# Kernel tuning notes

Measured on AMD Instinct MI355X. Metric: run time of the kernel, lower is better.

Reference implementation:

```python
import jax, jax.numpy as jnp
import numpy as np
from jax import lax

B, C_IN, H, W = 128, 3, 64, 64
HID = 128          # encoder hidden channels
D = 256            # embedding_dim
K = 1024           # codebook_size
COMMIT = 0.25      # commitment_cost


def conv(x, w, b, stride=2, pad=1):
    # x: NCHW, w: OIHW (torch Conv2d layout)
    y = lax.conv_general_dilated(x, w, (stride, stride), [(pad, pad), (pad, pad)],
                                 dimension_numbers=('NCHW', 'OIHW', 'NCHW'))
    return y + b[None, :, None, None]


def conv_t(x, w, b, stride=2, pad=1):
    # torch ConvTranspose2d: w is (in, out, kh, kw); equivalent to a conv with
    # lhs dilation = stride, flipped kernel, padding k-1-pad.
    k = w.shape[2]
    w_ = jnp.flip(w, (2, 3)).transpose(1, 0, 2, 3)  # -> (out, in, kh, kw)
    p = k - 1 - pad
    y = lax.conv_general_dilated(x, w_, (1, 1), [(p, p), (p, p)],
                                 lhs_dilation=(stride, stride),
                                 dimension_numbers=('NCHW', 'OIHW', 'NCHW'))
    return y + b[None, :, None, None]


def setup_inputs() -> dict:
    key = jax.random.key(0)
    ks = jax.random.split(key, 10)
    s = 0.05
    return {
        'x':        jax.random.normal(ks[0], (B, C_IN, H, W), jnp.float32),
        'enc_w1':   jax.random.normal(ks[1], (HID, C_IN, 4, 4), jnp.float32) * s,
        'enc_b1':   jnp.zeros((HID,), jnp.float32),
        'enc_w2':   jax.random.normal(ks[2], (D, HID, 4, 4), jnp.float32) * s,
        'enc_b2':   jnp.zeros((D,), jnp.float32),
        'dec_w1':   jax.random.normal(ks[3], (D, HID, 4, 4), jnp.float32) * s,   # ConvT: (in,out,kh,kw)
        'dec_b1':   jnp.zeros((HID,), jnp.float32),
        'dec_w2':   jax.random.normal(ks[4], (HID, C_IN, 4, 4), jnp.float32) * s,
        'dec_b2':   jnp.zeros((C_IN,), jnp.float32),
        'codebook': jax.random.normal(ks[5], (K, D), jnp.float32),  # embedding.weight.normal_()
    }


def vqvae_forward(x, enc_w1, enc_b1, enc_w2, enc_b2,
                  dec_w1, dec_b1, dec_w2, dec_b2, codebook):
    # ----- encoder -----
    h = jax.nn.relu(conv(x, enc_w1, enc_b1))          # (B, HID, 32, 32)
    e = conv(h, enc_w2, enc_b2)                        # (B, D, 16, 16)

    # ----- VectorQuantizerEMA.forward (eval mode, no mask) -----
    inputs = e.transpose(0, 2, 3, 1)                   # BCHW -> BHWC
    in_shape = inputs.shape
    flat = inputs.reshape(-1, D)                       # (N, D), N = B*16*16

    # squared L2 distances to every code: (N, K)
    dist = (jnp.sum(flat * flat, axis=1, keepdims=True)
            + jnp.sum(codebook * codebook, axis=1)
            - 2.0 * flat @ codebook.T)

    # max_one_hot(-distances) with straight-through gradients
    logits = -dist
    idx = jnp.argmax(logits, axis=-1)                  # (N,)
    oh = jax.nn.one_hot(idx, K, dtype=logits.dtype)
    flat_oh = oh + logits - lax.stop_gradient(logits)  # values == one-hot

    n_lat = in_shape[1] * in_shape[2]                  # H*W latents
    oh_encodings = flat_oh.reshape(in_shape[0], n_lat, K).transpose(0, 2, 1)  # (B, K, n)

    # quantize under no_grad (torch.no_grad block)
    quantized = lax.stop_gradient(flat_oh @ codebook).reshape(in_shape)

    e_latent_loss = jnp.mean((quantized - inputs) ** 2)
    loss = COMMIT * e_latent_loss

    # straight-through estimator
    quantized = inputs + lax.stop_gradient(quantized - inputs)

    avg_probs = jnp.mean(flat_oh, axis=0)
    perplexity = jnp.exp(-jnp.sum(avg_probs * jnp.log(avg_probs + 1e-10)))

    quantized_nchw = quantized.transpose(0, 3, 1, 2)   # BHWC -> BCHW

    # ----- decoder -----
    d1 = jax.nn.relu(conv_t(quantized_nchw, dec_w1, dec_b1))  # (B, HID, 32, 32)
    x_hat = conv_t(d1, dec_w2, dec_b2)                        # (B, 3, 64, 64)

    return x_hat, loss, perplexity, oh_encodings


def reference(x, enc_w1, enc_b1, enc_w2, enc_b2,
              dec_w1, dec_b1, dec_w2, dec_b2, codebook):
    return vqvae_forward(x, enc_w1, enc_b1, enc_w2, enc_b2,
                         dec_w1, dec_b1, dec_w2, dec_b2, codebook)
```

## Files before the change

### kernel.cpp

```cpp
#include <hip/hip_runtime.h>
#include <stdint.h>

#define NB   128
#define CIN  3
#define HID  128
#define DEM  256
#define KCB  1024
#define NLAT 32768

typedef __bf16 bf16x8 __attribute__((ext_vector_type(8)));
typedef _Float16 f16x8 __attribute__((ext_vector_type(8)));
typedef float  f32x4  __attribute__((ext_vector_type(4)));

__device__ inline unsigned short f2bf(float f) {
    unsigned u = __builtin_bit_cast(unsigned, f);
    u = (u + 0x7fff + ((u >> 16) & 1)) >> 16;
    return (unsigned short)u;
}

__global__ __launch_bounds__(256) void k_zero_oh(float* __restrict__ oh, int n4) {
    int t = blockIdx.x * 256 + threadIdx.x;
    f32x4 z = {0.f, 0.f, 0.f, 0.f};
    for (int i = t; i < n4; i += 256 * 2048)
        __builtin_nontemporal_store(z, (f32x4*)(oh + (size_t)i * 4));
}

__global__ __launch_bounds__(256) void k_conv1(const float* __restrict__ x,
        const float* __restrict__ w, const float* __restrict__ bias,
        unsigned short* __restrict__ hA) {
    __shared__ float sx[3][66][66];
    const int b = blockIdx.y;
    const int ocg = blockIdx.x;
    const int oc0 = ocg * 16;
    const int tid = threadIdx.x;
    for (int i = tid; i < 3 * 66 * 66; i += 256) ((float*)sx)[i] = 0.f;
    __syncthreads();
    const float* xb = x + (size_t)b * (3 * 64 * 64);
    for (int i = tid; i < 3 * 64 * 64; i += 256) {
        int ic = i >> 12; int rem = i & 4095; int y = rem >> 6; int xx = rem & 63;
        sx[ic][y + 1][xx + 1] = xb[i];
    }
    __syncthreads();
    for (int j = 0; j < 4; ++j) {
        int pos = tid + j * 256;
        int oy = pos >> 5, ox = pos & 31;
        float acc[16];
        #pragma unroll
        for (int i = 0; i < 16; ++i) acc[i] = 0.f;
        int iy0 = 2 * oy;
        int ix0 = 2 * ox;
        for (int ic = 0; ic < 3; ++ic) {
            float p[16];
            #pragma unroll
            for (int ky = 0; ky < 4; ++ky)
                #pragma unroll
                for (int kx = 0; kx < 4; ++kx)
                    p[ky * 4 + kx] = sx[ic][iy0 + ky][ix0 + kx];
            #pragma unroll
            for (int oc = 0; oc < 16; ++oc) {
                const float* wp = w + ((oc0 + oc) * 3 + ic) * 16;
                float a = acc[oc];
                #pragma unroll
                for (int t = 0; t < 16; ++t) a = fmaf(p[t], wp[t], a);
                acc[oc] = a;
            }
        }
        unsigned short rec[32];
        #pragma unroll
        for (int oc = 0; oc < 16; ++oc) {
            float v = acc[oc] + bias[oc0 + oc];
            v = v > 0.f ? v : 0.f;
            _Float16 hh = (_Float16)v;
            float hf = (float)hh;
            _Float16 ll = (_Float16)((v - hf) * 2048.0f);
            rec[oc] = __builtin_bit_cast(unsigned short, hh);
            rec[16 + oc] = __builtin_bit_cast(unsigned short, ll);
        }
        uint4* dst = (uint4*)(hA + ((size_t)(b * 8 + ocg) * 1024 + pos) * 32);
        uint4* r4 = (uint4*)rec;
        dst[0] = r4[0]; dst[1] = r4[1]; dst[2] = r4[2]; dst[3] = r4[3];
    }
}

__global__ void k_packwf(const float* __restrict__ w, unsigned short* __restrict__ wpf) {
    int t = blockIdx.x * 256 + threadIdx.x;
    int oc = t >> 7, rest = t & 127;
    int c0 = rest >> 4, ci = rest & 15;
    const float* src = w + ((size_t)(oc * 128 + c0 * 16 + ci)) * 16;
    float tv[16];
    #pragma unroll
    for (int i = 0; i < 16; i += 4) {
        float4 v = *(const float4*)(src + i);
        tv[i] = v.x; tv[i + 1] = v.y; tv[i + 2] = v.z; tv[i + 3] = v.w;
    }
    int g = oc >> 4, lr = oc & 15;
    #pragma unroll
    for (int ks = 0; ks < 8; ++ks) {
        int ky = ks >> 1, kxp = ks & 1;
        #pragma unroll
        for (int kxh = 0; kxh < 2; ++kxh) {
            float v = tv[ky * 4 + 2 * kxp + kxh];
            _Float16 hh = (_Float16)v;
            float hf = (float)hh;
            _Float16 ll = (_Float16)((v - hf) * 2048.0f);
            int d = kxh * 16 + ci;
            int hi = d >> 3, el = d & 7;
            size_t base = ((((size_t)(c0 * 8 + ks) * 16 + g) * 2 + 0) * 4 + hi) * 128 + lr * 8 + el;
            wpf[base]       = __builtin_bit_cast(unsigned short, hh);
            wpf[base + 512] = __builtin_bit_cast(unsigned short, ll);
        }
    }
}

__global__ __launch_bounds__(512) void k_conv2_mfma(const unsigned short* __restrict__ hA,
        const unsigned short* __restrict__ wpf, const float* __restrict__ bias,
        float* __restrict__ e) {
    __shared__ __attribute__((aligned(16))) unsigned short As[577 * 40];
    const int tid = threadIdx.x;
    const int b = blockIdx.y;
    const int ocg = blockIdx.x >> 1, yh = blockIdx.x & 1;
    const int lane = tid & 63, wv = tid >> 6;
    const int wm = wv >> 2, wn = wv & 3;
    const int lr = lane & 15, hi = lane >> 4;

    if (tid < 40) As[576 * 40 + tid] = 0;

    f32x4 acc0[4][2], acc1[4][2];
    #pragma unroll
    for (int i = 0; i < 4; ++i)
        #pragma unroll
        for (int j = 0; j < 2; ++j) {
            acc0[i][j] = (f32x4){0.f, 0.f, 0.f, 0.f};
            acc1[i][j] = (f32x4){0.f, 0.f, 0.f, 0.f};
        }

    for (int c0 = 0; c0 < 8; ++c0) {
        __syncthreads();
        {
            const size_t cbase = (size_t)(b * 8 + c0) * 1024;
            for (int p = tid; p < 2304; p += 512) {
                int l = p >> 7, rem = p & 127;
                int ixs = rem >> 2, q = rem & 3;
                int iy = yh * 16 - 1 + l;
                uint4* dst = (uint4*)(As + (l * 32 + (ixs & 1) * 16 + (ixs >> 1)) * 40 + q * 8);
                if (iy >= 0 && iy < 32)
                    *dst = *(const uint4*)(hA + (cbase + iy * 32 + ixs) * 32 + q * 8);
                else
                    *dst = (uint4){0u, 0u, 0u, 0u};
            }
        }
        __syncthreads();
        #pragma unroll
        for (int ks = 0; ks < 8; ++ks) {
            const int ky = ks >> 1, kxp = ks & 1;
            f16x8 bh[2], bl[2];
            #pragma unroll
            for (int nf = 0; nf < 2; ++nf) {
                const unsigned short* bp = wpf
                    + ((((size_t)(c0 * 8 + ks) * 16 + (ocg * 8 + wn * 2 + nf)) * 2 + 0) * 4 + hi) * 128 + lr * 8;
                bh[nf] = *(const f16x8*)bp;
                bl[nf] = *(const f16x8*)(bp + 512);
            }
            const int o = 2 * kxp - 1 + (hi >> 1);
            const int ix = 2 * lr + o;
            const bool xv = (ix >= 0) && (ix < 32);
            const int sbase = (o & 1) * 16 + (ix >> 1);
            #pragma unroll
            for (int mf = 0; mf < 4; ++mf) {
                int l = 2 * (wm * 4 + mf) + ky;
                int slot = xv ? (l * 32 + sbase) : 576;
                const unsigned short* ap = As + slot * 40 + (hi & 1) * 8;
                f16x8 a0 = *(const f16x8*)ap;
                f16x8 a1 = *(const f16x8*)(ap + 16);
                #pragma unroll
                for (int nf = 0; nf < 2; ++nf) {
                    acc0[mf][nf] = __builtin_amdgcn_mfma_f32_16x16x32_f16(a0, bh[nf], acc0[mf][nf], 0, 0, 0);
                    acc1[mf][nf] = __builtin_amdgcn_mfma_f32_16x16x32_f16(a0, bl[nf], acc1[mf][nf], 0, 0, 0);
                    acc1[mf][nf] = __builtin_amdgcn_mfma_f32_16x16x32_f16(a1, bh[nf], acc1[mf][nf], 0, 0, 0);
                }
            }
        }
    }
    #pragma unroll
    for (int mf = 0; mf < 4; ++mf) {
        int oy = yh * 8 + wm * 4 + mf;
        #pragma unroll
        for (int nf = 0; nf < 2; ++nf) {
            int oc = ocg * 128 + wn * 32 + nf * 16 + lr;
            float bv = bias[oc];
            #pragma unroll
            for (int r = 0; r < 4; ++r) {
                int ox = hi * 4 + r;
                size_t erow = (size_t)b * 256 + (size_t)oy * 16 + ox;
                e[erow * 256 + oc] = acc0[mf][nf][r] + acc1[mf][nf][r] * (1.0f / 2048.0f) + bv;
            }
        }
    }
}

__global__ void k_cnorm(const float* __restrict__ cb, float* __restrict__ cn) {
    int k = blockIdx.x * 256 + threadIdx.x;
    const float* cp = cb + (size_t)k * 256;
    float s = 0.f;
    #pragma unroll 8
    for (int d = 0; d < 256; d += 4) {
        float4 v = *(const float4*)(cp + d);
        s = fmaf(v.x, v.x, s); s = fmaf(v.y, v.y, s);
        s = fmaf(v.z, v.z, s); s = fmaf(v.w, v.w, s);
    }
    cn[k] = s;
}

__global__ void k_packcbp(const float* __restrict__ cb, unsigned short* __restrict__ cbp) {
    int t = blockIdx.x * 256 + threadIdx.x;
    int c = t >> 8, d = t & 255;
    float v = cb[(size_t)c * 256 + d];
    _Float16 hh = (_Float16)v;
    float hf = (float)hh;
    _Float16 ll = (_Float16)((v - hf) * 2048.0f);
    int g = c >> 4, lr = c & 15;
    int kq = d >> 5, rem = d & 31, hi = rem >> 3, el = rem & 7;
    size_t b0 = ((((size_t)(g * 8 + kq) * 2 + 0) * 4 + hi) * 16 + lr) * 8 + el;
    size_t b1 = ((((size_t)(g * 8 + kq) * 2 + 1) * 4 + hi) * 16 + lr) * 8 + el;
    cbp[b0] = __builtin_bit_cast(unsigned short, hh);
    cbp[b1] = __builtin_bit_cast(unsigned short, ll);
}

__global__ __launch_bounds__(512) void k_vq_mfma(const float* __restrict__ e,
        const unsigned short* __restrict__ cbp, const float* __restrict__ cn,
        const float* __restrict__ cb,
        int* __restrict__ idx, int* __restrict__ counts, float* __restrict__ sse,
        float* __restrict__ oh) {
    __shared__ __attribute__((aligned(16))) unsigned short As[64 * 520];
    __shared__ float redS[8][64];
    __shared__ int   redI[8][64];
    __shared__ int   winner[64];
    __shared__ float sred[64];
    const int tid = threadIdx.x;
    const int lane = tid & 63;
    const int wv = tid >> 6;
    const int lr = lane & 15, hi = lane >> 4;
    const int row0 = blockIdx.x * 64;

    {
        int row = tid >> 3, seg = tid & 7;
        const float* src = e + (size_t)(row0 + row) * 256 + seg * 32;
        unsigned short hb[32], lb[32];
        #pragma unroll
        for (int i = 0; i < 32; i += 4) {
            float4 v = *(const float4*)(src + i);
            float vv[4] = {v.x, v.y, v.z, v.w};
            #pragma unroll
            for (int q = 0; q < 4; ++q) {
                _Float16 hh = (_Float16)vv[q];
                float hf = (float)hh;
                _Float16 ll = (_Float16)((vv[q] - hf) * 2048.0f);
                hb[i + q] = __builtin_bit_cast(unsigned short, hh);
                lb[i + q] = __builtin_bit_cast(unsigned short, ll);
            }
        }
        uint4* dh = (uint4*)(As + row * 520 + seg * 32);
        uint4* dl = (uint4*)(As + row * 520 + 256 + seg * 32);
        #pragma unroll
        for (int u = 0; u < 4; ++u) { dh[u] = ((uint4*)hb)[u]; dl[u] = ((uint4*)lb)[u]; }
    }
    __syncthreads();

    float best_s[4][4];
    int   best_i[4][4];
    #pragma unroll
    for (int a = 0; a < 4; ++a)
        #pragma unroll
        for (int r = 0; r < 4; ++r) { best_s[a][r] = 3.4e38f; best_i[a][r] = 0; }

    for (int ph = 0; ph < 8; ++ph) {
        const int gidx = ph * 8 + wv;
        f32x4 acc0[4], acc1[4];
        #pragma unroll
        for (int i = 0; i < 4; ++i) {
            acc0[i] = (f32x4){0.f, 0.f, 0.f, 0.f};
            acc1[i] = (f32x4){0.f, 0.f, 0.f, 0.f};
        }
        #pragma unroll
        for (int kq = 0; kq < 8; ++kq) {
            const unsigned short* bp = cbp
                + (((size_t)(gidx * 8 + kq) * 2 + 0) * 4 + hi) * 128 + lr * 8;
            f16x8 bh = *(const f16x8*)bp;
            f16x8 bl = *(const f16x8*)(bp + 512);
            #pragma unroll
            for (int mf = 0; mf < 4; ++mf) {
                const unsigned short* ap = As + (mf * 16 + lr) * 520 + kq * 32 + hi * 8;
                f16x8 a0 = *(const f16x8*)ap;
                f16x8 a1 = *(const f16x8*)(ap + 256);
                acc0[mf] = __builtin_amdgcn_mfma_f32_16x16x32_f16(a0, bh, acc0[mf], 0, 0, 0);
                acc1[mf] = __builtin_amdgcn_mfma_f32_16x16x32_f16(a0, bl, acc1[mf], 0, 0, 0);
                acc1[mf] = __builtin_amdgcn_mfma_f32_16x16x32_f16(a1, bh, acc1[mf], 0, 0, 0);
            }
        }
        {
            int code = gidx * 16 + lr;
            float cnv = cn[code];
            #pragma unroll
            for (int mf = 0; mf < 4; ++mf)
                #pragma unroll
                for (int r = 0; r < 4; ++r) {
                    float dot = fmaf(acc1[mf][r], (1.0f / 2048.0f), acc0[mf][r]);
                    float s = fmaf(-2.0f, dot, cnv);
                    if (s < best_s[mf][r] || (s == best_s[mf][r] && code < best_i[mf][r])) {
                        best_s[mf][r] = s; best_i[mf][r] = code;
                    }
                }
        }
    }
    #pragma unroll
    for (int m = 1; m < 16; m <<= 1) {
        #pragma unroll
        for (int mf = 0; mf < 4; ++mf)
            #pragma unroll
            for (int r = 0; r < 4; ++r) {
                float os = __shfl_xor(best_s[mf][r], m, 64);
                int   oi = __shfl_xor(best_i[mf][r], m, 64);
                if (os < best_s[mf][r] || (os == best_s[mf][r] && oi < best_i[mf][r])) {
                    best_s[mf][r] = os; best_i[mf][r] = oi;
                }
            }
    }
    if (lr == 0) {
        #pragma unroll
        for (int mf = 0; mf < 4; ++mf)
            #pragma unroll
            for (int r = 0; r < 4; ++r) {
                int row = mf * 16 + hi * 4 + r;
                redS[wv][row] = best_s[mf][r];
                redI[wv][row] = best_i[mf][r];
            }
    }
    __syncthreads();
    if (tid < 64) {
        float bs = redS[0][tid]; int bi = redI[0][tid];
        for (int ww = 1; ww < 8; ++ww) {
            float s = redS[ww][tid]; int i2 = redI[ww][tid];
            if (s < bs || (s == bs && i2 < bi)) { bs = s; bi = i2; }
        }
        int rowg = row0 + tid;
        idx[rowg] = bi;
        atomicAdd(counts + bi, 1);
        int bimg = rowg >> 8, n = rowg & 255;
        __builtin_nontemporal_store(1.0f,
            oh + (size_t)bimg * (KCB * 256) + (size_t)bi * 256 + n);
        winner[tid] = bi;
    }
    __syncthreads();
    {
        int row = tid >> 3, seg = tid & 7;
        int bi = winner[row];
        const float* cp = cb + (size_t)bi * 256 + seg * 32;
        const float* ep = e + (size_t)(row0 + row) * 256 + seg * 32;
        float s = 0.f;
        #pragma unroll
        for (int i = 0; i < 32; i += 4) {
            float4 a = *(const float4*)(cp + i);
            float4 b = *(const float4*)(ep + i);
            float d0 = a.x - b.x, d1 = a.y - b.y, d2 = a.z - b.z, d3 = a.w - b.w;
            s = fmaf(d0, d0, s); s = fmaf(d1, d1, s);
            s = fmaf(d2, d2, s); s = fmaf(d3, d3, s);
        }
        s += __shfl_down(s, 4, 64);
        s += __shfl_down(s, 2, 64);
        s += __shfl_down(s, 1, 64);
        if ((tid & 7) == 0) sred[row] = s;
    }
    __syncthreads();
    if (tid == 0) {
        float t = 0.f;
        for (int i = 0; i < 64; ++i) t += sred[i];
        atomicAdd(sse, t);
    }
}

__global__ void k_cb2bf(const float* __restrict__ cb, unsigned short* __restrict__ cbb) {
    int t = blockIdx.x * 256 + threadIdx.x;
    float4 v = *(const float4*)(cb + (size_t)t * 4);
    ushort4 o;
    o.x = f2bf(v.x); o.y = f2bf(v.y); o.z = f2bf(v.z); o.w = f2bf(v.w);
    *(ushort4*)(cbb + (size_t)t * 4) = o;
}

__global__ void k_packw(const float* __restrict__ w, unsigned short* __restrict__ wp) {
    int t = blockIdx.x * 256 + threadIdx.x;
    int ci = t >> 7, oc = t & 127;
    const float* src = w + ((size_t)ci * 128 + oc) * 16;
    float tv[16];
    #pragma unroll
    for (int i = 0; i < 16; i += 4) {
        float4 v = *(const float4*)(src + i);
        tv[i] = v.x; tv[i + 1] = v.y; tv[i + 2] = v.z; tv[i + 3] = v.w;
    }
    #pragma unroll
    for (int p = 0; p < 4; ++p) {
        int a = p >> 1, b2 = p & 1;
        #pragma unroll
        for (int tap = 0; tap < 4; ++tap) {
            int dy = tap >> 1, dx = tap & 1;
            float v = tv[((1 - a) + 2 * dy) * 4 + (1 - b2) + 2 * dx];
            wp[((((p * 4 + tap) * 128) + oc) << 8) + ci] = f2bf(v);
        }
    }
}

__global__ void k_packw2t(const float* __restrict__ w, unsigned short* __restrict__ wt) {
    int t = blockIdx.x * 256 + threadIdx.x;
    int el = t & 7, lr = (t >> 3) & 15, hi = (t >> 7) & 3;
    int cig = (t >> 9) & 3, tp = (t >> 11) & 3, p = (t >> 13) & 3;
    int ci = cig * 32 + hi * 8 + el;
    int a = p >> 1, bb = p & 1;
    int ky0 = 1 - a, kx0 = 1 - bb;
    int wtap;
    if (tp == 0) wtap = ky0 * 4 + kx0;
    else if (tp == 1) wtap = ky0 * 4 + kx0 + 2;
    else if (tp == 2) wtap = (ky0 + 2) * 4 + kx0;
    else wtap = (ky0 + 2) * 4 + kx0 + 2;
    unsigned short v = 0;
    if (lr < 3) v = f2bf(w[((size_t)ci * 3 + lr) * 16 + wtap]);
    wt[t] = v;
}

__global__ __launch_bounds__(512) void k_convt1_mfma(const int* __restrict__ idx,
        const unsigned short* __restrict__ cbb, const unsigned short* __restrict__ wp,
        const float* __restrict__ bias, unsigned short* __restrict__ d1b) {
    __shared__ unsigned short As[257 * 72];
    __shared__ unsigned short Bs[128 * 72];
    __shared__ int sidx[256];
    const int tid = threadIdx.x;
    const int b  = blockIdx.y;
    const int p  = blockIdx.x;
    const int a  = p >> 1, bb2 = p & 1;
    if (tid < 256) sidx[tid] = idx[b * 256 + tid] * 256;
    if (tid < 72)  As[256 * 72 + tid] = 0;
    const int lane = tid & 63;
    const int w    = tid >> 6;
    const int wm = w >> 2, wn = w & 3;
    const int lr = lane & 15, hi = lane >> 4;
    const int koff = hi * 8;
    f32x4 acc[8][2];
    #pragma unroll
    for (int i = 0; i < 8; ++i)
        #pragma unroll
        for (int j = 0; j < 2; ++j) acc[i][j] = (f32x4){0.f, 0.f, 0.f, 0.f};

    for (int c0 = 0; c0 < 256; c0 += 64) {
        for (int tap = 0; tap < 4; ++tap) {
            __syncthreads();
            if (tap == 0) {
                int row = tid >> 1, half = tid & 1;
                const uint4* src = (const uint4*)(cbb + sidx[row] + c0 + half * 32);
                uint4 v0 = src[0], v1 = src[1], v2 = src[2], v3 = src[3];
                uint4* dst = (uint4*)(As + row * 72 + half * 32);
                dst[0] = v0; dst[1] = v1; dst[2] = v2; dst[3] = v3;
            }
            {
                int oc = tid >> 2, q = tid & 3;
                const uint4* src = (const uint4*)(wp + (((p * 4 + tap) * 128 + oc) << 8) + c0 + q * 16);
                uint4 v0 = src[0], v1 = src[1];
                uint4* dst = (uint4*)(Bs + oc * 72 + q * 16);
                dst[0] = v0; dst[1] = v1;
            }
            __syncthreads();
            const int dy = tap >> 1, dx = tap & 1;
            const int xo = lr + bb2 - dx;
            const bool xv = (xo >= 0) && (xo < 16);
            #pragma unroll
            for (int kk = 0; kk < 2; ++kk) {
                bf16x8 aF[8];
                #pragma unroll
                for (int i = 0; i < 8; ++i) {
                    int typ = wm * 8 + i + a - dy;
                    int row = (xv && typ >= 0 && typ < 16) ? typ * 16 + xo : 256;
                    aF[i] = *(const bf16x8*)(As + row * 72 + kk * 32 + koff);
                }
                #pragma unroll
                for (int j = 0; j < 2; ++j) {
                    bf16x8 bF = *(const bf16x8*)(Bs + ((wn * 2 + j) * 16 + lr) * 72 + kk * 32 + koff);
                    #pragma unroll
                    for (int i = 0; i < 8; ++i)
                        acc[i][j] = __builtin_amdgcn_mfma_f32_16x16x32_bf16(aF[i], bF, acc[i][j], 0, 0, 0);
                }
            }
        }
    }
    #pragma unroll
    for (int j = 0; j < 2; ++j) {
        int oc = (wn * 2 + j) * 16 + lr;
        float bv = bias[oc];
        #pragma unroll
        for (int i = 0; i < 8; ++i) {
            int mt = wm * 8 + i;
            int oy = 2 * mt + a;
            #pragma unroll
            for (int r = 0; r < 4; ++r) {
                int ox = bb2 + 2 * (hi * 4 + r);
                float v = acc[i][j][r] + bv;
                v = v > 0.f ? v : 0.f;
                d1b[(((size_t)b * 32 + oy) * 32 + ox) * 128 + oc] = f2bf(v);
            }
        }
    }
}

__global__ __launch_bounds__(512) void k_convt2_mfma(const unsigned short* __restrict__ d1b,
        const unsigned short* __restrict__ wt, const float* __restrict__ bias,
        float* __restrict__ xhat) {
    __shared__ __attribute__((aligned(16))) unsigned short sd[18 * 34 * 32];
    const int tid = threadIdx.x;
    const int b = blockIdx.y;
    const int p = blockIdx.x >> 1, yh = blockIdx.x & 1;
    const int a = p >> 1, bb = p & 1;
    const int lane = tid & 63, wv = tid >> 6;
    const int lr = lane & 15, hi = lane >> 4;

    f32x4 acc[4];
    #pragma unroll
    for (int i = 0; i < 4; ++i) acc[i] = (f32x4){0.f, 0.f, 0.f, 0.f};

    for (int cig = 0; cig < 4; ++cig) {
        __syncthreads();
        for (int q4 = tid; q4 < 2448; q4 += 512) {
            int l = q4 / 136, rem = q4 % 136, xx = rem >> 2, q = rem & 3;
            int iy = yh * 16 - 1 + l, ixx = xx - 1;
            uint4* dst = (uint4*)(sd + (l * 34 + xx) * 32 + q * 8);
            if (iy >= 0 && iy < 32 && ixx >= 0 && ixx < 32)
                *dst = *(const uint4*)(d1b + (((size_t)b * 32 + iy) * 32 + ixx) * 128 + cig * 32 + q * 8);
            else
                *dst = (uint4){0u, 0u, 0u, 0u};
        }
        __syncthreads();
        #pragma unroll
        for (int tp = 0; tp < 4; ++tp) {
            const unsigned short* bp = wt + ((((p * 4 + tp) * 4 + cig) * 4 + hi) * 16 + lr) * 8;
            bf16x8 bF = *(const bf16x8*)bp;
            #pragma unroll
            for (int mf = 0; mf < 4; ++mf) {
                int pos = wv * 64 + mf * 16 + lr;
                int myl = pos >> 5, mx = pos & 31;
                int l = myl + a + (tp < 2 ? 1 : 0);
                int xx = mx + bb + ((tp & 1) ? 0 : 1);
                bf16x8 aF = *(const bf16x8*)(sd + (l * 34 + xx) * 32 + hi * 8);
                acc[mf] = __builtin_amdgcn_mfma_f32_16x16x32_bf16(aF, bF, acc[mf], 0, 0, 0);
            }
        }
    }
    if (lr < 3) {
        float bv = bias[lr];
        #pragma unroll
        for (int mf = 0; mf < 4; ++mf) {
            #pragma unroll
            for (int r = 0; r < 4; ++r) {
                int pos = wv * 64 + mf * 16 + hi * 4 + r;
                int oy = 2 * (yh * 16 + (pos >> 5)) + a;
                int ox = 2 * (pos & 31) + bb;
                xhat[(((size_t)b * 3 + lr) * 64 + oy) * 64 + ox] = acc[mf][r] + bv;
            }
        }
    }
}

__global__ void k_final(const int* __restrict__ counts, const float* __restrict__ sse,
                        float* __restrict__ out_loss, float* __restrict__ out_perp) {
    __shared__ float red[256];
    int tid = threadIdx.x;
    float s = 0.f;
    for (int k = tid; k < 1024; k += 256) {
        float p = (float)counts[k] * (1.f / 32768.f);
        s += p * logf(p + 1e-10f);
    }
    red[tid] = s;
    __syncthreads();
    for (int st = 128; st > 0; st >>= 1) {
        if (tid < st) red[tid] += red[tid + st];
        __syncthreads();
    }
    if (tid == 0) {
        *out_perp = expf(-red[0]);
        *out_loss = 0.25f * (*sse) / 8388608.0f;
    }
}

extern "C" void kernel_launch(void* const* d_in, const int* in_sizes, int n_in,
                              void* d_out, int out_size, void* d_ws, size_t ws_size,
                              hipStream_t stream) {
    const float* x   = (const float*)d_in[0];
    const float* ew1 = (const float*)d_in[1];
    const float* eb1 = (const float*)d_in[2];
    const float* ew2 = (const float*)d_in[3];
    const float* eb2 = (const float*)d_in[4];
    const float* dw1 = (const float*)d_in[5];
    const float* db1 = (const float*)d_in[6];
    const float* dw2 = (const float*)d_in[7];
    const float* db2 = (const float*)d_in[8];
    const float* cb  = (const float*)d_in[9];

    float* out  = (float*)d_out;
    float* xhat = out;
    float* loss = out + 1572864;
    float* perp = out + 1572865;
    float* oh   = out + 1572866;

    char* ws = (char*)d_ws;
    unsigned short* hA = (unsigned short*)ws;
    float* e      = (float*)(ws + (size_t)64 * 1024 * 1024);
    int*   idx    = (int*)(ws + (size_t)96 * 1024 * 1024);
    int*   counts = idx + NLAT;
    float* sse    = (float*)(counts + KCB);
    float* cn     = sse + 1;
    unsigned short* cbp = (unsigned short*)ws;
    unsigned short* d1b = (unsigned short*)ws;
    unsigned short* cbb = (unsigned short*)e;
    unsigned short* wpk = (unsigned short*)(ws + (size_t)65 * 1024 * 1024);
    unsigned short* wt  = (unsigned short*)(ws + (size_t)67 * 1024 * 1024);
    unsigned short* wpf = (unsigned short*)(((uintptr_t)oh + 15) & ~(uintptr_t)15);

    hipMemsetAsync(counts, 0, KCB * 4 + 4, stream);

    k_cnorm<<<4, 256, 0, stream>>>(cb, cn);
    k_packwf<<<128, 256, 0, stream>>>(ew2, wpf);
    k_conv1<<<dim3(8, 128), 256, 0, stream>>>(x, ew1, eb1, hA);
    k_zero_oh<<<2048, 256, 0, stream>>>(oh + 524304, (33554432 - 524304) / 4);
    k_conv2_mfma<<<dim3(4, 128), 512, 0, stream>>>(hA, wpf, eb2, e);
    k_zero_oh<<<64, 256, 0, stream>>>(oh, 524304 / 4);
    k_packcbp<<<1024, 256, 0, stream>>>(cb, cbp);
    k_vq_mfma<<<512, 512, 0, stream>>>(e, cbp, cn, cb, idx, counts, sse, oh);
    k_cb2bf<<<256, 256, 0, stream>>>(cb, cbb);
    k_packw<<<128, 256, 0, stream>>>(dw1, wpk);
    k_packw2t<<<128, 256, 0, stream>>>(dw2, wt);
    k_convt1_mfma<<<dim3(4, 128), 512, 0, stream>>>(idx, cbb, wpk, db1, d1b);
    k_convt2_mfma<<<dim3(8, 128), 512, 0, stream>>>(d1b, wt, db2, xhat);
    k_final<<<1, 256, 0, stream>>>(counts, sse, loss, perp);
}
```

Baseline: 618.8 us.

## Double VQ block row tile to 128 and reduce argmin per phase via LDS

The VQ distance kernel now handles 128 latent rows per block instead of 64, so each codebook fragment loaded from global memory feeds twice as many MFMAs and half as many blocks are launched. Because per-row best-score registers would double, the argmin is instead reduced across lanes with shuffles after every phase and merged into shared-memory running minima. This adds shuffle and LDS work per phase and doubles LDS use to about 133KB. It also leaves only 256 blocks, which may underfill the GPU's compute units.

```diff
diff --git a/kernel.cpp b/kernel.cpp
--- a/kernel.cpp
+++ b/kernel.cpp
@@ -231,19 +231,20 @@
         const float* __restrict__ cb,
         int* __restrict__ idx, int* __restrict__ counts, float* __restrict__ sse,
         float* __restrict__ oh) {
-    __shared__ __attribute__((aligned(16))) unsigned short As[64 * 520];
-    __shared__ float redS[8][64];
-    __shared__ int   redI[8][64];
-    __shared__ int   winner[64];
-    __shared__ float sred[64];
+    __shared__ __attribute__((aligned(16))) unsigned short As[128 * 520];
+    __shared__ float redS[8][128];
+    __shared__ int   redI[8][128];
+    __shared__ int   winner[128];
+    __shared__ float sred[128];
     const int tid = threadIdx.x;
     const int lane = tid & 63;
     const int wv = tid >> 6;
     const int lr = lane & 15, hi = lane >> 4;
-    const int row0 = blockIdx.x * 64;
-
-    {
-        int row = tid >> 3, seg = tid & 7;
+    const int row0 = blockIdx.x * 128;
+
+    #pragma unroll
+    for (int rr = 0; rr < 2; ++rr) {
+        int row = rr * 64 + (tid >> 3), seg = tid & 7;
         const float* src = e + (size_t)(row0 + row) * 256 + seg * 32;
         unsigned short hb[32], lb[32];
         #pragma unroll
@@ -264,20 +265,18 @@
         #pragma unroll
         for (int u = 0; u < 4; ++u) { dh[u] = ((uint4*)hb)[u]; dl[u] = ((uint4*)lb)[u]; }
     }
+    for (int i = tid; i < 8 * 128; i += 512) {
+        redS[i >> 7][i & 127] = 3.4e38f;
+        redI[i >> 7][i & 127] = 0;
+    }
     __syncthreads();
-
-    float best_s[4][4];
-    int   best_i[4][4];
-    #pragma unroll
-    for (int a = 0; a < 4; ++a)
-        #pragma unroll
-        for (int r = 0; r < 4; ++r) { best_s[a][r] = 3.4e38f; best_i[a][r] = 0; }
 
     for (int ph = 0; ph < 8; ++ph) {
         const int gidx = ph * 8 + wv;
-        f32x4 acc0[4], acc1[4];
-        #pragma unroll
-        for (int i = 0; i < 4; ++i) {
+        const int code = gidx * 16 + lr;
+        f32x4 acc0[8], acc1[8];
+        #pragma unroll
+        for (int i = 0; i < 8; ++i) {
             acc0[i] = (f32x4){0.f, 0.f, 0.f, 0.f};
             acc1[i] = (f32x4){0.f, 0.f, 0.f, 0.f};
         }
@@ -288,7 +287,7 @@
             f16x8 bh = *(const f16x8*)bp;
             f16x8 bl = *(const f16x8*)(bp + 512);
             #pragma unroll
-            for (int mf = 0; mf < 4; ++mf) {
+            for (int mf = 0; mf < 8; ++mf) {
                 const unsigned short* ap = As + (mf * 16 + lr) * 520 + kq * 32 + hi * 8;
                 f16x8 a0 = *(const f16x8*)ap;
                 f16x8 a1 = *(const f16x8*)(ap + 256);
@@ -297,46 +296,39 @@
                 acc1[mf] = __builtin_amdgcn_mfma_f32_16x16x32_f16(a1, bh, acc1[mf], 0, 0, 0);
             }
         }
-        {
-            int code = gidx * 16 + lr;
-            float cnv = cn[code];
-            #pragma unroll
-            for (int mf = 0; mf < 4; ++mf)
+        const float cnv = cn[code];
+        #pragma unroll
+        for (int mf = 0; mf < 8; ++mf) {
+            float ps[4]; int pi[4];
+            #pragma unroll
+            for (int r = 0; r < 4; ++r) {
+                float dot = fmaf(acc1[mf][r], (1.0f / 2048.0f), acc0[mf][r]);
+                ps[r] = fmaf(-2.0f, dot, cnv);
+                pi[r] = code;
+            }
+            #pragma unroll
+            for (int m = 1; m < 16; m <<= 1) {
                 #pragma unroll
                 for (int r = 0; r < 4; ++r) {
-                    float dot = fmaf(acc1[mf][r], (1.0f / 2048.0f), acc0[mf][r]);
-                    float s = fmaf(-2.0f, dot, cnv);
-                    if (s < best_s[mf][r] || (s == best_s[mf][r] && code < best_i[mf][r])) {
-                        best_s[mf][r] = s; best_i[mf][r] = code;
+                    float os = __shfl_xor(ps[r], m, 64);
+                    int   oi = __shfl_xor(pi[r], m, 64);
+                    if (os < ps[r] || (os == ps[r] && oi < pi[r])) { ps[r] = os; pi[r] = oi; }
+                }
+            }
+            if (lr == 0) {
+                #pragma unroll
+                for (int r = 0; r < 4; ++r) {
+                    int row = mf * 16 + hi * 4 + r;
+                    float cs = redS[wv][row]; int ci2 = redI[wv][row];
+                    if (ps[r] < cs || (ps[r] == cs && pi[r] < ci2)) {
+                        redS[wv][row] = ps[r]; redI[wv][row] = pi[r];
                     }
                 }
-        }
-    }
-    #pragma unroll
-    for (int m = 1; m < 16; m <<= 1) {
-        #pragma unroll
-        for (int mf = 0; mf < 4; ++mf)
-            #pragma unroll
-            for (int r = 0; r < 4; ++r) {
-                float os = __shfl_xor(best_s[mf][r], m, 64);
-                int   oi = __shfl_xor(best_i[mf][r], m, 64);
-                if (os < best_s[mf][r] || (os == best_s[mf][r] && oi < best_i[mf][r])) {
-                    best_s[mf][r] = os; best_i[mf][r] = oi;
-                }
-            }
-    }
-    if (lr == 0) {
-        #pragma unroll
-        for (int mf = 0; mf < 4; ++mf)
-            #pragma unroll
-            for (int r = 0; r < 4; ++r) {
-                int row = mf * 16 + hi * 4 + r;
-                redS[wv][row] = best_s[mf][r];
-                redI[wv][row] = best_i[mf][r];
-            }
+            }
+        }
     }
     __syncthreads();
-    if (tid < 64) {
+    if (tid < 128) {
         float bs = redS[0][tid]; int bi = redI[0][tid];
         for (int ww = 1; ww < 8; ++ww) {
             float s = redS[ww][tid]; int i2 = redI[ww][tid];
@@ -352,28 +344,27 @@
     }
     __syncthreads();
     {
-        int row = tid >> 3, seg = tid & 7;
+        int row = tid >> 2, seg = tid & 3;
         int bi = winner[row];
-        const float* cp = cb + (size_t)bi * 256 + seg * 32;
-        const float* ep = e + (size_t)(row0 + row) * 256 + seg * 32;
+        const float* cp = cb + (size_t)bi * 256 + seg * 64;
+        const float* ep = e + (size_t)(row0 + row) * 256 + seg * 64;
         float s = 0.f;
         #pragma unroll
-        for (int i = 0; i < 32; i += 4) {
+        for (int i = 0; i < 64; i += 4) {
             float4 a = *(const float4*)(cp + i);
             float4 b = *(const float4*)(ep + i);
             float d0 = a.x - b.x, d1 = a.y - b.y, d2 = a.z - b.z, d3 = a.w - b.w;
             s = fmaf(d0, d0, s); s = fmaf(d1, d1, s);
             s = fmaf(d2, d2, s); s = fmaf(d3, d3, s);
         }
-        s += __shfl_down(s, 4, 64);
         s += __shfl_down(s, 2, 64);
         s += __shfl_down(s, 1, 64);
-        if ((tid & 7) == 0) sred[row] = s;
+        if ((tid & 3) == 0) sred[row] = s;
     }
     __syncthreads();
     if (tid == 0) {
         float t = 0.f;
-        for (int i = 0; i < 64; ++i) t += sred[i];
+        for (int i = 0; i < 128; ++i) t += sred[i];
         atomicAdd(sse, t);
     }
 }
@@ -628,7 +619,7 @@
     k_conv2_mfma<<<dim3(4, 128), 512, 0, stream>>>(hA, wpf, eb2, e);
     k_zero_oh<<<64, 256, 0, stream>>>(oh, 524304 / 4);
     k_packcbp<<<1024, 256, 0, stream>>>(cb, cbp);
-    k_vq_mfma<<<512, 512, 0, stream>>>(e, cbp, cn, cb, idx, counts, sse, oh);
+    k_vq_mfma<<<256, 512, 0, stream>>>(e, cbp, cn, cb, idx, counts, sse, oh);
     k_cb2bf<<<256, 256, 0, stream>>>(cb, cbb);
     k_packw<<<128, 256, 0, stream>>>(dw1, wpk);
     k_packw2t<<<128, 256, 0, stream>>>(dw2, wt);
```

Result: slower. 868.5 us, median of 2 (+40.3%).
